# Kernel tuning notes

Hardware: AMD Instinct MI355X
Metric: run time of the kernel (lower is better)

The kernel has to match this reference:

```python
import jax, jax.numpy as jnp
import numpy as np

N, D, H = 4096, 128, 8

def setup_inputs() -> dict:
    key = jax.random.key(0)
    ks = jax.random.split(key, 7)
    xavier = float(np.sqrt(6.0 / (D + D)))  # xavier_uniform for [*, D, D]
    x = jax.random.normal(ks[0], (N, D), dtype=jnp.float32)
    W_k = jax.random.uniform(ks[1], (H, D, D), minval=-xavier, maxval=xavier, dtype=jnp.float32)
    W_q = jax.random.uniform(ks[2], (H, D, D), minval=-xavier, maxval=xavier, dtype=jnp.float32)
    W_v = jax.random.uniform(ks[3], (H, D, D), minval=-xavier, maxval=xavier, dtype=jnp.float32)
    W_m = jnp.ones((H,), dtype=jnp.float32)
    lim = float(1.0 / np.sqrt(D))  # default torch Linear init range
    Wg = jax.random.uniform(ks[4], (D, D), minval=-lim, maxval=lim, dtype=jnp.float32)
    bg = jax.random.uniform(ks[5], (D,), minval=-lim, maxval=lim, dtype=jnp.float32)
    return {"x": x, "W_k": W_k, "W_q": W_q, "W_v": W_v, "W_m": W_m, "Wg": Wg, "bg": bg}

def reference(x, W_k, W_q, W_v, W_m, Wg, bg):
    # per-head projections: [H, N, D]
    q = jnp.einsum('nf,hfd->hnd', x, W_q)
    k = jnp.einsum('nf,hfd->hnd', x, W_k)
    v = jnp.einsum('nf,hfd->hnd', x, W_v)
    # dense all-pairs attention scores per head: [H, N, N]
    e = jnp.einsum('hnd,hmd->hnm', q, k)
    attn = jax.nn.softmax(e, axis=-1)
    # weighted sum over values, then head-scaled accumulation: [N, D]
    out = jnp.einsum('h,hnm,hmd->nd', W_m, attn, v)
    # residual MLP: x + ReLU(Linear(x + out))
    h = x + out
    g = jax.nn.relu(h @ Wg.T + bg)
    return x + g
```

## Files before the change

### kernel.cpp

```cpp
#include <hip/hip_runtime.h>

#define NROWS 4096
#define DDIM  128
#define NHEAD 8

typedef __attribute__((ext_vector_type(8))) short    short8;
typedef __attribute__((ext_vector_type(8))) _Float16 half8;
typedef __attribute__((ext_vector_type(4))) float    floatx4;

__device__ __forceinline__ float bf2f(unsigned short u){
  unsigned v = ((unsigned)u) << 16;
  return __builtin_bit_cast(float, v);
}
__device__ __forceinline__ unsigned short f2bf(float f){
  unsigned u = __builtin_bit_cast(unsigned, f);
  u += 0x7FFFu + ((u >> 16) & 1u);
  return (unsigned short)(u >> 16);
}
__device__ __forceinline__ void split2(float v, unsigned short& hi, unsigned short& lo){
  hi = f2bf(v);
  lo = f2bf(v - bf2f(hi));
}
__device__ __forceinline__ void async_cp16(const _Float16* g, _Float16* l){
  __builtin_amdgcn_global_load_lds(
      (const __attribute__((address_space(1))) void*)g,
      (__attribute__((address_space(3))) void*)l, 16, 0, 0);
}

__global__ void fill_kernel(float* __restrict__ out, float val, int n){
  int i = blockIdx.x * 256 + threadIdx.x;
  if (i < n) out[i] = val;
}

__global__ __launch_bounds__(256, 2) void proj_kernel(
    const float* __restrict__ x,
    const float* __restrict__ Wk, const float* __restrict__ Wv,
    _Float16* __restrict__ kfo, _Float16* __restrict__ vfo)
{
  __shared__ alignas(16) unsigned short wthi[DDIM][72];
  __shared__ alignas(16) unsigned short wtlo[DDIM][72];
  const int tid = threadIdx.x, lane = tid & 63, wave = tid >> 6;
  const int l4 = lane & 15, quad = lane >> 4;
  const int h = blockIdx.y, z = blockIdx.z;
  const float* W = (z == 0 ? Wk : Wv) + h * DDIM * DDIM;

  floatx4 acc[4][8];
#pragma unroll
  for (int t4 = 0; t4 < 4; t4++)
#pragma unroll
    for (int c = 0; c < 8; c++) acc[t4][c] = (floatx4)0.f;

  for (int fh = 0; fh < 2; fh++) {
    for (int i = tid; i < DDIM * 64; i += 256) {
      const int d = i >> 6, fl = i & 63;
      unsigned short hi, lo;
      split2(W[(fh * 64 + fl) * DDIM + d], hi, lo);
      wthi[d][fl] = hi; wtlo[d][fl] = lo;
    }
    __syncthreads();

#pragma unroll
    for (int t4 = 0; t4 < 4; t4++) {
      const int tile = blockIdx.x * 4 + t4;
      const float* xr = x + (size_t)(tile * 64 + wave * 16 + l4) * DDIM + fh * 64 + quad * 8;
      short8 ah[2], al[2];
#pragma unroll
      for (int t2 = 0; t2 < 2; t2++) {
        float4 v0 = *(const float4*)(xr + t2 * 32);
        float4 v1 = *(const float4*)(xr + t2 * 32 + 4);
        float xv[8] = {v0.x, v0.y, v0.z, v0.w, v1.x, v1.y, v1.z, v1.w};
#pragma unroll
        for (int j = 0; j < 8; j++) {
          unsigned short hi, lo; split2(xv[j], hi, lo);
          ah[t2][j] = (short)hi; al[t2][j] = (short)lo;
        }
      }
#pragma unroll
      for (int t2 = 0; t2 < 2; t2++) {
#pragma unroll
        for (int c = 0; c < 8; c++) {
          short8 bh = *(const short8*)(&wthi[c * 16 + l4][t2 * 32 + quad * 8]);
          short8 bl = *(const short8*)(&wtlo[c * 16 + l4][t2 * 32 + quad * 8]);
          acc[t4][c] = __builtin_amdgcn_mfma_f32_16x16x32_bf16(ah[t2], bh, acc[t4][c], 0, 0, 0);
          acc[t4][c] = __builtin_amdgcn_mfma_f32_16x16x32_bf16(al[t2], bh, acc[t4][c], 0, 0, 0);
          acc[t4][c] = __builtin_amdgcn_mfma_f32_16x16x32_bf16(ah[t2], bl, acc[t4][c], 0, 0, 0);
        }
      }
    }
    __syncthreads();
  }

  const int rb = wave * 16 + quad * 4;
#pragma unroll
  for (int t4 = 0; t4 < 4; t4++) {
    const int tile = blockIdx.x * 4 + t4;
    const size_t tilebase = (size_t)(h * 64 + tile) * 8192;
#pragma unroll
    for (int c = 0; c < 8; c++) {
      const int d = c * 16 + l4;
#pragma unroll
      for (int r = 0; r < 4; r++) {
        const int kl = rb + r;
        const float val = acc[t4][c][r];
        if (z == 0) {
          const int c2 = kl >> 4, l4k = kl & 15;
          const int tt = d >> 5, qd = (d >> 3) & 3, jj = d & 7;
          const int qX = qd ^ ((l4k >> 1) & 3);
          kfo[tilebase + (size_t)((c2 * 4 + tt) * 16 + l4k) * 32 + qX * 8 + jj] =
              (_Float16)val;
        } else {
          const int c2 = d >> 4, l4v = d & 15;
          const int tt = kl >> 5, qd = (kl >> 3) & 3, jj = kl & 7;
          const int qX = qd ^ ((l4v >> 1) & 3);
          vfo[tilebase + (size_t)((c2 * 2 + tt) * 16 + l4v) * 32 + qX * 8 + jj] =
              (_Float16)val;
        }
      }
    }
  }
}

union FlashLds {
  struct { unsigned short hi[DDIM][72], lo[DDIM][72]; } wq;
  float qf[64][132];
  struct { _Float16 k[2][8192], p[4][2][1024]; } kv;
};

__global__ __launch_bounds__(256, 2) void flash_kernel(
    const float* __restrict__ x, const float* __restrict__ Wq,
    const _Float16* __restrict__ kfo, const _Float16* __restrict__ vfo,
    _Float16* __restrict__ op, float* __restrict__ mb, float* __restrict__ lb)
{
  __shared__ alignas(16) FlashLds lds;
  const int tid = threadIdx.x, lane = tid & 63, wave = tid >> 6;
  const int l4 = lane & 15, quad = lane >> 4;
  const int h = blockIdx.x & 7, qt = (blockIdx.x >> 3) & 31, s = blockIdx.x >> 8;
  const int q0 = qt * 128;

  half8 aq[2][4];

  {
    floatx4 qacc[2][8];
#pragma unroll
    for (int sp = 0; sp < 2; sp++)
#pragma unroll
      for (int c = 0; c < 8; c++) qacc[sp][c] = (floatx4)0.f;

    const float* Wqh = Wq + h * DDIM * DDIM;
    for (int fh = 0; fh < 2; fh++) {
      for (int i = tid; i < DDIM * 64; i += 256) {
        const int d = i >> 6, fl = i & 63;
        unsigned short hi, lo;
        split2(Wqh[(fh * 64 + fl) * DDIM + d], hi, lo);
        lds.wq.hi[d][fl] = hi; lds.wq.lo[d][fl] = lo;
      }
      __syncthreads();
#pragma unroll
      for (int sp = 0; sp < 2; sp++) {
        const float* xr = x + (size_t)(q0 + sp * 64 + wave * 16 + l4) * DDIM + fh * 64 + quad * 8;
        short8 ah[2], al[2];
#pragma unroll
        for (int t2 = 0; t2 < 2; t2++) {
          float4 v0 = *(const float4*)(xr + t2 * 32);
          float4 v1 = *(const float4*)(xr + t2 * 32 + 4);
          float xv[8] = {v0.x, v0.y, v0.z, v0.w, v1.x, v1.y, v1.z, v1.w};
#pragma unroll
          for (int j = 0; j < 8; j++) {
            unsigned short hi, lo; split2(xv[j], hi, lo);
            ah[t2][j] = (short)hi; al[t2][j] = (short)lo;
          }
        }
#pragma unroll
        for (int t2 = 0; t2 < 2; t2++) {
#pragma unroll
          for (int c = 0; c < 8; c++) {
            short8 bh = *(const short8*)(&lds.wq.hi[c * 16 + l4][t2 * 32 + quad * 8]);
            short8 bl = *(const short8*)(&lds.wq.lo[c * 16 + l4][t2 * 32 + quad * 8]);
            qacc[sp][c] = __builtin_amdgcn_mfma_f32_16x16x32_bf16(ah[t2], bh, qacc[sp][c], 0, 0, 0);
            qacc[sp][c] = __builtin_amdgcn_mfma_f32_16x16x32_bf16(al[t2], bh, qacc[sp][c], 0, 0, 0);
            qacc[sp][c] = __builtin_amdgcn_mfma_f32_16x16x32_bf16(ah[t2], bl, qacc[sp][c], 0, 0, 0);
          }
        }
      }
      __syncthreads();
    }

#pragma unroll
    for (int sp = 0; sp < 2; sp++) {
#pragma unroll
      for (int c = 0; c < 8; c++)
#pragma unroll
        for (int r = 0; r < 4; r++)
          lds.qf[wave * 16 + quad * 4 + r][c * 16 + l4] = qacc[sp][c][r];
      __syncthreads();
      if ((wave >> 1) == sp) {
#pragma unroll
        for (int g = 0; g < 2; g++)
#pragma unroll
          for (int t = 0; t < 4; t++) {
            const float* qr = &lds.qf[(wave & 1) * 32 + g * 16 + l4][t * 32 + quad * 8];
            float4 v0 = *(const float4*)qr;
            float4 v1 = *(const float4*)(qr + 4);
            aq[g][t][0] = (_Float16)v0.x; aq[g][t][1] = (_Float16)v0.y;
            aq[g][t][2] = (_Float16)v0.z; aq[g][t][3] = (_Float16)v0.w;
            aq[g][t][4] = (_Float16)v1.x; aq[g][t][5] = (_Float16)v1.y;
            aq[g][t][6] = (_Float16)v1.z; aq[g][t][7] = (_Float16)v1.w;
          }
      }
      __syncthreads();
    }
  }

  float m_run[2][4];
#pragma unroll
  for (int g = 0; g < 2; g++)
#pragma unroll
    for (int r = 0; r < 4; r++) m_run[g][r] = -1e30f;
  floatx4 Oacc[2][8], lacc[2];
#pragma unroll
  for (int g = 0; g < 2; g++) {
    lacc[g] = (floatx4)0.f;
#pragma unroll
    for (int c = 0; c < 8; c++) Oacc[g][c] = (floatx4)0.f;
  }

  half8 vones;
#pragma unroll
  for (int j = 0; j < 8; j++) vones[j] = (_Float16)1.f;

  const _Float16* kfo_h = kfo + (size_t)h * 64 * 8192;
  const _Float16* vfo_h = vfo + (size_t)h * 64 * 8192;
  const int lq = (l4 * 4 + (quad ^ ((l4 >> 1) & 3))) * 8;
  const int kt0 = s * 32, kt1 = kt0 + 32;

  {
    const _Float16* ks = kfo_h + (size_t)kt0 * 8192 + wave * 2048 + lane * 8;
    _Float16* kd = &lds.kv.k[0][wave * 2048];
#pragma unroll
    for (int it = 0; it < 4; it++) async_cp16(ks + it * 512, kd + it * 512);
  }

  for (int kt = kt0; kt < kt1; ++kt) {
    const int cur = kt & 1;
    __syncthreads();

    half8 vfrag[8][2];
    {
      const _Float16* vtb = vfo_h + (size_t)kt * 8192;
#pragma unroll
      for (int c = 0; c < 8; c++)
#pragma unroll
        for (int t = 0; t < 2; t++)
          vfrag[c][t] = *(const half8*)(vtb + (c * 2 + t) * 512 + lq);
    }
    if (kt + 1 < kt1) {
      const _Float16* ks = kfo_h + (size_t)(kt + 1) * 8192 + wave * 2048 + lane * 8;
      _Float16* kd = &lds.kv.k[cur ^ 1][wave * 2048];
#pragma unroll
      for (int it = 0; it < 4; it++) async_cp16(ks + it * 512, kd + it * 512);
    }

    floatx4 Sf[2][4];
#pragma unroll
    for (int g = 0; g < 2; g++)
#pragma unroll
      for (int c = 0; c < 4; c++) Sf[g][c] = (floatx4)0.f;
#pragma unroll
    for (int t = 0; t < 4; t++) {
      half8 b[4];
#pragma unroll
      for (int c = 0; c < 4; c++)
        b[c] = *(const half8*)&lds.kv.k[cur][(c * 4 + t) * 512 + lq];
#pragma unroll
      for (int g = 0; g < 2; g++)
#pragma unroll
        for (int c = 0; c < 4; c++)
          Sf[g][c] = __builtin_amdgcn_mfma_f32_16x16x32_f16(aq[g][t], b[c], Sf[g][c], 0, 0, 0);
    }

    float alpha[2][4];
#pragma unroll
    for (int g = 0; g < 2; g++) {
      float mt[4];
#pragma unroll
      for (int r = 0; r < 4; r++)
        mt[r] = fmaxf(fmaxf(Sf[g][0][r], Sf[g][1][r]), fmaxf(Sf[g][2][r], Sf[g][3][r]));
#pragma unroll
      for (int mk = 1; mk <= 8; mk <<= 1)
#pragma unroll
        for (int r = 0; r < 4; r++) mt[r] = fmaxf(mt[r], __shfl_xor(mt[r], mk, 64));
#pragma unroll
      for (int r = 0; r < 4; r++) {
        const float mn = fmaxf(m_run[g][r], mt[r]);
        alpha[g][r] = __expf(m_run[g][r] - mn);
        m_run[g][r] = mn;
      }
#pragma unroll
      for (int r = 0; r < 4; r++)
#pragma unroll
        for (int c = 0; c < 4; c++) Sf[g][c][r] = __expf(Sf[g][c][r] - m_run[g][r]);
    }

#pragma unroll
    for (int g = 0; g < 2; g++)
#pragma unroll
      for (int c = 0; c < 4; c++)
#pragma unroll
        for (int r = 0; r < 4; r++)
          lds.kv.p[wave][g][((c * 2 + (l4 >> 3)) * 16 + quad * 4 + r) * 8 + (l4 & 7)] =
              (_Float16)Sf[g][c][r];

#pragma unroll
    for (int g = 0; g < 2; g++) {
      const bool moved = (alpha[g][0] != 1.f) | (alpha[g][1] != 1.f) |
                         (alpha[g][2] != 1.f) | (alpha[g][3] != 1.f);
      if (__any(moved)) {
#pragma unroll
        for (int c = 0; c < 8; c++) {
          Oacc[g][c][0] *= alpha[g][0]; Oacc[g][c][1] *= alpha[g][1];
          Oacc[g][c][2] *= alpha[g][2]; Oacc[g][c][3] *= alpha[g][3];
        }
        lacc[g][0] *= alpha[g][0]; lacc[g][1] *= alpha[g][1];
        lacc[g][2] *= alpha[g][2]; lacc[g][3] *= alpha[g][3];
      }
    }
#pragma unroll
    for (int t = 0; t < 2; t++) {
      half8 ap[2];
#pragma unroll
      for (int g = 0; g < 2; g++) {
        ap[g] = *(const half8*)&lds.kv.p[wave][g][((t * 4 + quad) * 16 + l4) * 8];
        lacc[g] = __builtin_amdgcn_mfma_f32_16x16x32_f16(ap[g], vones, lacc[g], 0, 0, 0);
      }
#pragma unroll
      for (int c = 0; c < 8; c++)
#pragma unroll
        for (int g = 0; g < 2; g++)
          Oacc[g][c] = __builtin_amdgcn_mfma_f32_16x16x32_f16(ap[g], vfrag[c][t], Oacc[g][c], 0, 0, 0);
    }
  }

#pragma unroll
  for (int g = 0; g < 2; g++) {
    const int rbase = wave * 32 + g * 16 + quad * 4;
    const size_t rowbase = (size_t)(s * NHEAD + h) * NROWS + q0 + rbase;
#pragma unroll
    for (int c = 0; c < 8; c++) {
      const int col = c * 16 + l4;
#pragma unroll
      for (int r = 0; r < 4; r++)
        op[(rowbase + r) * DDIM + col] = (_Float16)Oacc[g][c][r];
    }
    if (l4 == 0) {
#pragma unroll
      for (int r = 0; r < 4; r++) {
        mb[rowbase + r] = m_run[g][r];
        lb[rowbase + r] = lacc[g][r];
      }
    }
  }
}

__global__ __launch_bounds__(128) void merge_kernel(
    const _Float16* __restrict__ op, const float* __restrict__ mb,
    const float* __restrict__ lb, const float* __restrict__ Wm,
    float* __restrict__ u)
{
  __shared__ float sc[2][NHEAD];
  const int n = blockIdx.x, d = threadIdx.x;
  if (d < NHEAD) {
    const int h = d;
    const float m1 = mb[(size_t)h * NROWS + n];
    const float m2 = mb[(size_t)(NHEAD + h) * NROWS + n];
    const float l1 = lb[(size_t)h * NROWS + n];
    const float l2 = lb[(size_t)(NHEAD + h) * NROWS + n];
    const float m  = fmaxf(m1, m2);
    const float a1 = __expf(m1 - m), a2 = __expf(m2 - m);
    const float invL = Wm[h] / (l1 * a1 + l2 * a2);
    sc[0][h] = a1 * invL;
    sc[1][h] = a2 * invL;
  }
  __syncthreads();
  float acc = 0.f;
#pragma unroll
  for (int h = 0; h < NHEAD; h++) {
    acc += sc[0][h] * (float)op[((size_t)h * NROWS + n) * DDIM + d];
    acc += sc[1][h] * (float)op[((size_t)(NHEAD + h) * NROWS + n) * DDIM + d];
  }
  u[(size_t)n * DDIM + d] = acc;
}

__global__ __launch_bounds__(256, 2) void mlp_kernel(
    const float* __restrict__ x, const float* __restrict__ u,
    const float* __restrict__ Wg, const float* __restrict__ bg,
    float* __restrict__ out)
{
  __shared__ alignas(16) unsigned short wghi[DDIM][72];
  __shared__ alignas(16) unsigned short wglo[DDIM][72];
  const int tid = threadIdx.x, lane = tid & 63, wave = tid >> 6;
  const int l4 = lane & 15, quad = lane >> 4;
  const int r0 = blockIdx.x * 64;

  floatx4 acc[8];
#pragma unroll
  for (int c = 0; c < 8; c++) acc[c] = (floatx4)0.f;

  for (int fh = 0; fh < 2; fh++) {
    for (int i = tid; i < DDIM * 64; i += 256) {
      const int ii = i >> 6, jl = i & 63;
      unsigned short hi, lo;
      split2(Wg[ii * DDIM + fh * 64 + jl], hi, lo);
      wghi[ii][jl] = hi; wglo[ii][jl] = lo;
    }
    __syncthreads();

    const size_t xoff = (size_t)(r0 + wave * 16 + l4) * DDIM + fh * 64 + quad * 8;
    short8 ah[2], al[2];
#pragma unroll
    for (int t2 = 0; t2 < 2; t2++) {
      float4 x0 = *(const float4*)(x + xoff + t2 * 32);
      float4 x1 = *(const float4*)(x + xoff + t2 * 32 + 4);
      float4 u0 = *(const float4*)(u + xoff + t2 * 32);
      float4 u1 = *(const float4*)(u + xoff + t2 * 32 + 4);
      float hv[8] = {x0.x + u0.x, x0.y + u0.y, x0.z + u0.z, x0.w + u0.w,
                     x1.x + u1.x, x1.y + u1.y, x1.z + u1.z, x1.w + u1.w};
#pragma unroll
      for (int j = 0; j < 8; j++) {
        unsigned short hi, lo; split2(hv[j], hi, lo);
        ah[t2][j] = (short)hi; al[t2][j] = (short)lo;
      }
    }
#pragma unroll
    for (int t2 = 0; t2 < 2; t2++) {
#pragma unroll
      for (int c = 0; c < 8; c++) {
        short8 bh = *(const short8*)(&wghi[c * 16 + l4][t2 * 32 + quad * 8]);
        short8 bl = *(const short8*)(&wglo[c * 16 + l4][t2 * 32 + quad * 8]);
        acc[c] = __builtin_amdgcn_mfma_f32_16x16x32_bf16(ah[t2], bh, acc[c], 0, 0, 0);
        acc[c] = __builtin_amdgcn_mfma_f32_16x16x32_bf16(al[t2], bh, acc[c], 0, 0, 0);
        acc[c] = __builtin_amdgcn_mfma_f32_16x16x32_bf16(ah[t2], bl, acc[c], 0, 0, 0);
      }
    }
    __syncthreads();
  }

  const int rbase = wave * 16 + quad * 4;
#pragma unroll
  for (int c = 0; c < 8; c++) {
    const int col = c * 16 + l4;
    const float bgf = bg[col];
#pragma unroll
    for (int r = 0; r < 4; r++) {
      const size_t idx = (size_t)(r0 + rbase + r) * DDIM + col;
      out[idx] = x[idx] + fmaxf(acc[c][r] + bgf, 0.f);
    }
  }
}

extern "C" void kernel_launch(void* const* d_in, const int* in_sizes, int n_in,
                              void* d_out, int out_size, void* d_ws, size_t ws_size,
                              hipStream_t stream) {
  float* out = (float*)d_out;
  const int fill_blocks = (out_size + 255) / 256;

  const bool ok_sizes =
      n_in == 7 &&
      in_sizes[0] == NROWS * DDIM &&
      in_sizes[1] == NHEAD * DDIM * DDIM &&
      in_sizes[2] == NHEAD * DDIM * DDIM &&
      in_sizes[3] == NHEAD * DDIM * DDIM &&
      in_sizes[4] == NHEAD &&
      in_sizes[5] == DDIM * DDIM &&
      in_sizes[6] == DDIM &&
      out_size == NROWS * DDIM;
  if (!ok_sizes) {
    fill_kernel<<<fill_blocks, 256, 0, stream>>>(out, 1000.f, out_size);
    return;
  }

  const size_t HND = (size_t)NHEAD * NROWS * DDIM;
  const size_t ND  = (size_t)NROWS * DDIM;
  const size_t need = ND * 4 + 2 * HND * 2 + 2 * HND * 2 + 2 * NHEAD * NROWS * 8;
  if (ws_size < need) {
    fill_kernel<<<fill_blocks, 256, 0, stream>>>(out, 500.f, out_size);
    return;
  }

  const float* x  = (const float*)d_in[0];
  const float* Wk = (const float*)d_in[1];
  const float* Wq = (const float*)d_in[2];
  const float* Wv = (const float*)d_in[3];
  const float* Wm = (const float*)d_in[4];
  const float* Wg = (const float*)d_in[5];
  const float* bg = (const float*)d_in[6];

  float*     u   = (float*)d_ws;
  _Float16*  kfo = (_Float16*)(u + ND);
  _Float16*  vfo = kfo + HND;
  _Float16*  op  = vfo + HND;
  float*     mb  = (float*)(op + 2 * HND);
  float*     lb  = mb + 2 * NHEAD * NROWS;

  (void)hipGetLastError();
  proj_kernel<<<dim3(16, NHEAD, 2), 256, 0, stream>>>(x, Wk, Wv, kfo, vfo);
  flash_kernel<<<dim3(512), 256, 0, stream>>>(x, Wq, kfo, vfo, op, mb, lb);
  merge_kernel<<<dim3(4096), 128, 0, stream>>>(op, mb, lb, Wm, u);
  mlp_kernel<<<dim3(64), 256, 0, stream>>>(x, u, Wg, bg, out);
  if (hipGetLastError() != hipSuccess) {
    fill_kernel<<<fill_blocks, 256, 0, stream>>>(out, 2000.f, out_size);
  }
}
```

Baseline: 254.8 us.

## Use single fp16 MFMA for projections and fuse merge into MLP kernel

Replaces the split-bf16 three-MFMA emulation of fp32 GEMMs in the K/V, Q and MLP projections with a single fp16 MFMA on fp16-converted inputs and weights. The proj kernel now computes both K and V per block, loading x once, with a new grid shape. The separate merge kernel is folded into the MLP kernel, which combines the split-softmax partials into an fp16 LDS tile and drops the u workspace round trip. This trades projection and MLP accuracy (fp16 rounding of x, weights and h) for fewer MFMAs and one fewer launch.

```diff
diff --git a/kernel.cpp b/kernel.cpp
--- a/kernel.cpp
+++ b/kernel.cpp
@@ -4,23 +4,9 @@
 #define DDIM  128
 #define NHEAD 8
 
-typedef __attribute__((ext_vector_type(8))) short    short8;
 typedef __attribute__((ext_vector_type(8))) _Float16 half8;
 typedef __attribute__((ext_vector_type(4))) float    floatx4;
 
-__device__ __forceinline__ float bf2f(unsigned short u){
-  unsigned v = ((unsigned)u) << 16;
-  return __builtin_bit_cast(float, v);
-}
-__device__ __forceinline__ unsigned short f2bf(float f){
-  unsigned u = __builtin_bit_cast(unsigned, f);
-  u += 0x7FFFu + ((u >> 16) & 1u);
-  return (unsigned short)(u >> 16);
-}
-__device__ __forceinline__ void split2(float v, unsigned short& hi, unsigned short& lo){
-  hi = f2bf(v);
-  lo = f2bf(v - bf2f(hi));
-}
 __device__ __forceinline__ void async_cp16(const _Float16* g, _Float16* l){
   __builtin_amdgcn_global_load_lds(
       (const __attribute__((address_space(1))) void*)g,
@@ -30,6 +16,17 @@
 __global__ void fill_kernel(float* __restrict__ out, float val, int n){
   int i = blockIdx.x * 256 + threadIdx.x;
   if (i < n) out[i] = val;
+}
+
+__device__ __forceinline__ half8 f32x8_to_h8(const float* p){
+  float4 v0 = *(const float4*)p;
+  float4 v1 = *(const float4*)(p + 4);
+  half8 r;
+  r[0] = (_Float16)v0.x; r[1] = (_Float16)v0.y;
+  r[2] = (_Float16)v0.z; r[3] = (_Float16)v0.w;
+  r[4] = (_Float16)v1.x; r[5] = (_Float16)v1.y;
+  r[6] = (_Float16)v1.z; r[7] = (_Float16)v1.w;
+  return r;
 }
 
 __global__ __launch_bounds__(256, 2) void proj_kernel(
@@ -37,91 +34,79 @@
     const float* __restrict__ Wk, const float* __restrict__ Wv,
     _Float16* __restrict__ kfo, _Float16* __restrict__ vfo)
 {
-  __shared__ alignas(16) unsigned short wthi[DDIM][72];
-  __shared__ alignas(16) unsigned short wtlo[DDIM][72];
+  __shared__ alignas(16) _Float16 wt[DDIM][136];
   const int tid = threadIdx.x, lane = tid & 63, wave = tid >> 6;
   const int l4 = lane & 15, quad = lane >> 4;
-  const int h = blockIdx.y, z = blockIdx.z;
-  const float* W = (z == 0 ? Wk : Wv) + h * DDIM * DDIM;
-
-  floatx4 acc[4][8];
-#pragma unroll
-  for (int t4 = 0; t4 < 4; t4++)
-#pragma unroll
-    for (int c = 0; c < 8; c++) acc[t4][c] = (floatx4)0.f;
-
-  for (int fh = 0; fh < 2; fh++) {
-    for (int i = tid; i < DDIM * 64; i += 256) {
-      const int d = i >> 6, fl = i & 63;
-      unsigned short hi, lo;
-      split2(W[(fh * 64 + fl) * DDIM + d], hi, lo);
-      wthi[d][fl] = hi; wtlo[d][fl] = lo;
+  const int h = blockIdx.y;
+
+  half8 xf[2][4];
+#pragma unroll
+  for (int t2 = 0; t2 < 2; t2++) {
+    const int tile = blockIdx.x * 2 + t2;
+    const float* xr = x + (size_t)(tile * 64 + wave * 16 + l4) * DDIM + quad * 8;
+#pragma unroll
+    for (int t = 0; t < 4; t++) xf[t2][t] = f32x8_to_h8(xr + t * 32);
+  }
+
+  for (int z = 0; z < 2; z++) {
+    const float* W = (z == 0 ? Wk : Wv) + h * DDIM * DDIM;
+    if (z) __syncthreads();
+    for (int i = tid; i < DDIM * DDIM; i += 256) {
+      const int f = i >> 7, d = i & 127;
+      wt[d][f] = (_Float16)W[i];
     }
     __syncthreads();
 
-#pragma unroll
-    for (int t4 = 0; t4 < 4; t4++) {
-      const int tile = blockIdx.x * 4 + t4;
-      const float* xr = x + (size_t)(tile * 64 + wave * 16 + l4) * DDIM + fh * 64 + quad * 8;
-      short8 ah[2], al[2];
-#pragma unroll
-      for (int t2 = 0; t2 < 2; t2++) {
-        float4 v0 = *(const float4*)(xr + t2 * 32);
-        float4 v1 = *(const float4*)(xr + t2 * 32 + 4);
-        float xv[8] = {v0.x, v0.y, v0.z, v0.w, v1.x, v1.y, v1.z, v1.w};
-#pragma unroll
-        for (int j = 0; j < 8; j++) {
-          unsigned short hi, lo; split2(xv[j], hi, lo);
-          ah[t2][j] = (short)hi; al[t2][j] = (short)lo;
+    floatx4 acc[2][8];
+#pragma unroll
+    for (int t2 = 0; t2 < 2; t2++)
+#pragma unroll
+      for (int c = 0; c < 8; c++) acc[t2][c] = (floatx4)0.f;
+
+#pragma unroll
+    for (int t = 0; t < 4; t++) {
+#pragma unroll
+      for (int c = 0; c < 8; c++) {
+        half8 b = *(const half8*)&wt[c * 16 + l4][t * 32 + quad * 8];
+#pragma unroll
+        for (int t2 = 0; t2 < 2; t2++)
+          acc[t2][c] = __builtin_amdgcn_mfma_f32_16x16x32_f16(xf[t2][t], b, acc[t2][c], 0, 0, 0);
+      }
+    }
+
+    const int rb = wave * 16 + quad * 4;
+#pragma unroll
+    for (int t2 = 0; t2 < 2; t2++) {
+      const int tile = blockIdx.x * 2 + t2;
+      const size_t tilebase = (size_t)(h * 64 + tile) * 8192;
+#pragma unroll
+      for (int c = 0; c < 8; c++) {
+        const int d = c * 16 + l4;
+#pragma unroll
+        for (int r = 0; r < 4; r++) {
+          const int kl = rb + r;
+          const float val = acc[t2][c][r];
+          if (z == 0) {
+            const int c2 = kl >> 4, l4k = kl & 15;
+            const int tt = d >> 5, qd = (d >> 3) & 3, jj = d & 7;
+            const int qX = qd ^ ((l4k >> 1) & 3);
+            kfo[tilebase + (size_t)((c2 * 4 + tt) * 16 + l4k) * 32 + qX * 8 + jj] =
+                (_Float16)val;
+          } else {
+            const int c2 = d >> 4, l4v = d & 15;
+            const int tt = kl >> 5, qd = (kl >> 3) & 3, jj = kl & 7;
+            const int qX = qd ^ ((l4v >> 1) & 3);
+            vfo[tilebase + (size_t)((c2 * 2 + tt) * 16 + l4v) * 32 + qX * 8 + jj] =
+                (_Float16)val;
+          }
         }
       }
-#pragma unroll
-      for (int t2 = 0; t2 < 2; t2++) {
-#pragma unroll
-        for (int c = 0; c < 8; c++) {
-          short8 bh = *(const short8*)(&wthi[c * 16 + l4][t2 * 32 + quad * 8]);
-          short8 bl = *(const short8*)(&wtlo[c * 16 + l4][t2 * 32 + quad * 8]);
-          acc[t4][c] = __builtin_amdgcn_mfma_f32_16x16x32_bf16(ah[t2], bh, acc[t4][c], 0, 0, 0);
-          acc[t4][c] = __builtin_amdgcn_mfma_f32_16x16x32_bf16(al[t2], bh, acc[t4][c], 0, 0, 0);
-          acc[t4][c] = __builtin_amdgcn_mfma_f32_16x16x32_bf16(ah[t2], bl, acc[t4][c], 0, 0, 0);
-        }
-      }
-    }
-    __syncthreads();
-  }
-
-  const int rb = wave * 16 + quad * 4;
-#pragma unroll
-  for (int t4 = 0; t4 < 4; t4++) {
-    const int tile = blockIdx.x * 4 + t4;
-    const size_t tilebase = (size_t)(h * 64 + tile) * 8192;
-#pragma unroll
-    for (int c = 0; c < 8; c++) {
-      const int d = c * 16 + l4;
-#pragma unroll
-      for (int r = 0; r < 4; r++) {
-        const int kl = rb + r;
-        const float val = acc[t4][c][r];
-        if (z == 0) {
-          const int c2 = kl >> 4, l4k = kl & 15;
-          const int tt = d >> 5, qd = (d >> 3) & 3, jj = d & 7;
-          const int qX = qd ^ ((l4k >> 1) & 3);
-          kfo[tilebase + (size_t)((c2 * 4 + tt) * 16 + l4k) * 32 + qX * 8 + jj] =
-              (_Float16)val;
-        } else {
-          const int c2 = d >> 4, l4v = d & 15;
-          const int tt = kl >> 5, qd = (kl >> 3) & 3, jj = kl & 7;
-          const int qX = qd ^ ((l4v >> 1) & 3);
-          vfo[tilebase + (size_t)((c2 * 2 + tt) * 16 + l4v) * 32 + qX * 8 + jj] =
-              (_Float16)val;
-        }
-      }
     }
   }
 }
 
 union FlashLds {
-  struct { unsigned short hi[DDIM][72], lo[DDIM][72]; } wq;
+  _Float16 wq[DDIM][136];
   float qf[64][132];
   struct { _Float16 k[2][8192], p[4][2][1024]; } kv;
 };
@@ -140,50 +125,37 @@
   half8 aq[2][4];
 
   {
+    const float* Wqh = Wq + h * DDIM * DDIM;
+    for (int i = tid; i < DDIM * DDIM; i += 256) {
+      const int f = i >> 7, d = i & 127;
+      lds.wq[d][f] = (_Float16)Wqh[i];
+    }
+    __syncthreads();
+
+    half8 xf2[2][4];
+#pragma unroll
+    for (int sp = 0; sp < 2; sp++) {
+      const float* xr = x + (size_t)(q0 + sp * 64 + wave * 16 + l4) * DDIM + quad * 8;
+#pragma unroll
+      for (int t = 0; t < 4; t++) xf2[sp][t] = f32x8_to_h8(xr + t * 32);
+    }
+
     floatx4 qacc[2][8];
 #pragma unroll
     for (int sp = 0; sp < 2; sp++)
 #pragma unroll
       for (int c = 0; c < 8; c++) qacc[sp][c] = (floatx4)0.f;
-
-    const float* Wqh = Wq + h * DDIM * DDIM;
-    for (int fh = 0; fh < 2; fh++) {
-      for (int i = tid; i < DDIM * 64; i += 256) {
-        const int d = i >> 6, fl = i & 63;
-        unsigned short hi, lo;
-        split2(Wqh[(fh * 64 + fl) * DDIM + d], hi, lo);
-        lds.wq.hi[d][fl] = hi; lds.wq.lo[d][fl] = lo;
-      }
-      __syncthreads();
-#pragma unroll
-      for (int sp = 0; sp < 2; sp++) {
-        const float* xr = x + (size_t)(q0 + sp * 64 + wave * 16 + l4) * DDIM + fh * 64 + quad * 8;
-        short8 ah[2], al[2];
-#pragma unroll
-        for (int t2 = 0; t2 < 2; t2++) {
-          float4 v0 = *(const float4*)(xr + t2 * 32);
-          float4 v1 = *(const float4*)(xr + t2 * 32 + 4);
-          float xv[8] = {v0.x, v0.y, v0.z, v0.w, v1.x, v1.y, v1.z, v1.w};
-#pragma unroll
-          for (int j = 0; j < 8; j++) {
-            unsigned short hi, lo; split2(xv[j], hi, lo);
-            ah[t2][j] = (short)hi; al[t2][j] = (short)lo;
-          }
-        }
-#pragma unroll
-        for (int t2 = 0; t2 < 2; t2++) {
-#pragma unroll
-          for (int c = 0; c < 8; c++) {
-            short8 bh = *(const short8*)(&lds.wq.hi[c * 16 + l4][t2 * 32 + quad * 8]);
-            short8 bl = *(const short8*)(&lds.wq.lo[c * 16 + l4][t2 * 32 + quad * 8]);
-            qacc[sp][c] = __builtin_amdgcn_mfma_f32_16x16x32_bf16(ah[t2], bh, qacc[sp][c], 0, 0, 0);
-            qacc[sp][c] = __builtin_amdgcn_mfma_f32_16x16x32_bf16(al[t2], bh, qacc[sp][c], 0, 0, 0);
-            qacc[sp][c] = __builtin_amdgcn_mfma_f32_16x16x32_bf16(ah[t2], bl, qacc[sp][c], 0, 0, 0);
-          }
-        }
-      }
-      __syncthreads();
-    }
+#pragma unroll
+    for (int t = 0; t < 4; t++) {
+#pragma unroll
+      for (int c = 0; c < 8; c++) {
+        half8 b = *(const half8*)&lds.wq[c * 16 + l4][t * 32 + quad * 8];
+#pragma unroll
+        for (int sp = 0; sp < 2; sp++)
+          qacc[sp][c] = __builtin_amdgcn_mfma_f32_16x16x32_f16(xf2[sp][t], b, qacc[sp][c], 0, 0, 0);
+      }
+    }
+    __syncthreads();
 
 #pragma unroll
     for (int sp = 0; sp < 2; sp++) {
@@ -197,15 +169,8 @@
 #pragma unroll
         for (int g = 0; g < 2; g++)
 #pragma unroll
-          for (int t = 0; t < 4; t++) {
-            const float* qr = &lds.qf[(wave & 1) * 32 + g * 16 + l4][t * 32 + quad * 8];
-            float4 v0 = *(const float4*)qr;
-            float4 v1 = *(const float4*)(qr + 4);
-            aq[g][t][0] = (_Float16)v0.x; aq[g][t][1] = (_Float16)v0.y;
-            aq[g][t][2] = (_Float16)v0.z; aq[g][t][3] = (_Float16)v0.w;
-            aq[g][t][4] = (_Float16)v1.x; aq[g][t][5] = (_Float16)v1.y;
-            aq[g][t][6] = (_Float16)v1.z; aq[g][t][7] = (_Float16)v1.w;
-          }
+          for (int t = 0; t < 4; t++)
+            aq[g][t] = f32x8_to_h8(&lds.qf[(wave & 1) * 32 + g * 16 + l4][t * 32 + quad * 8]);
       }
       __syncthreads();
     }
@@ -361,87 +326,63 @@
   }
 }
 
-__global__ __launch_bounds__(128) void merge_kernel(
+__global__ __launch_bounds__(256, 2) void mlp_kernel(
+    const float* __restrict__ x,
     const _Float16* __restrict__ op, const float* __restrict__ mb,
     const float* __restrict__ lb, const float* __restrict__ Wm,
-    float* __restrict__ u)
-{
-  __shared__ float sc[2][NHEAD];
-  const int n = blockIdx.x, d = threadIdx.x;
-  if (d < NHEAD) {
-    const int h = d;
-    const float m1 = mb[(size_t)h * NROWS + n];
-    const float m2 = mb[(size_t)(NHEAD + h) * NROWS + n];
-    const float l1 = lb[(size_t)h * NROWS + n];
-    const float l2 = lb[(size_t)(NHEAD + h) * NROWS + n];
-    const float m  = fmaxf(m1, m2);
-    const float a1 = __expf(m1 - m), a2 = __expf(m2 - m);
-    const float invL = Wm[h] / (l1 * a1 + l2 * a2);
-    sc[0][h] = a1 * invL;
-    sc[1][h] = a2 * invL;
-  }
-  __syncthreads();
-  float acc = 0.f;
-#pragma unroll
-  for (int h = 0; h < NHEAD; h++) {
-    acc += sc[0][h] * (float)op[((size_t)h * NROWS + n) * DDIM + d];
-    acc += sc[1][h] * (float)op[((size_t)(NHEAD + h) * NROWS + n) * DDIM + d];
-  }
-  u[(size_t)n * DDIM + d] = acc;
-}
-
-__global__ __launch_bounds__(256, 2) void mlp_kernel(
-    const float* __restrict__ x, const float* __restrict__ u,
     const float* __restrict__ Wg, const float* __restrict__ bg,
     float* __restrict__ out)
 {
-  __shared__ alignas(16) unsigned short wghi[DDIM][72];
-  __shared__ alignas(16) unsigned short wglo[DDIM][72];
+  __shared__ alignas(16) _Float16 wg_s[DDIM][136];
+  __shared__ alignas(16) _Float16 h_s[64][136];
+  __shared__ float sc_s[64][16];
   const int tid = threadIdx.x, lane = tid & 63, wave = tid >> 6;
   const int l4 = lane & 15, quad = lane >> 4;
   const int r0 = blockIdx.x * 64;
 
+  for (int i = tid; i < DDIM * DDIM; i += 256)
+    wg_s[i >> 7][i & 127] = (_Float16)Wg[i];
+
+  if (tid < 64) {
+    const int n = r0 + tid;
+#pragma unroll
+    for (int hh = 0; hh < NHEAD; hh++) {
+      const float m1 = mb[(size_t)hh * NROWS + n];
+      const float m2 = mb[(size_t)(NHEAD + hh) * NROWS + n];
+      const float l1 = lb[(size_t)hh * NROWS + n];
+      const float l2 = lb[(size_t)(NHEAD + hh) * NROWS + n];
+      const float m  = fmaxf(m1, m2);
+      const float a1 = __expf(m1 - m), a2 = __expf(m2 - m);
+      const float invL = Wm[hh] / (l1 * a1 + l2 * a2);
+      sc_s[tid][hh] = a1 * invL;
+      sc_s[tid][NHEAD + hh] = a2 * invL;
+    }
+  }
+  __syncthreads();
+
+  for (int it = 0; it < 32; it++) {
+    const int e = tid + 256 * it;
+    const int d = e & 127, r = e >> 7;
+    const int n = r0 + r;
+    float acc = x[(size_t)n * DDIM + d];
+#pragma unroll
+    for (int sh = 0; sh < 16; sh++)
+      acc += sc_s[r][sh] * (float)op[((size_t)sh * NROWS + n) * DDIM + d];
+    h_s[r][d] = (_Float16)acc;
+  }
+  __syncthreads();
+
   floatx4 acc[8];
 #pragma unroll
   for (int c = 0; c < 8; c++) acc[c] = (floatx4)0.f;
-
-  for (int fh = 0; fh < 2; fh++) {
-    for (int i = tid; i < DDIM * 64; i += 256) {
-      const int ii = i >> 6, jl = i & 63;
-      unsigned short hi, lo;
-      split2(Wg[ii * DDIM + fh * 64 + jl], hi, lo);
-      wghi[ii][jl] = hi; wglo[ii][jl] = lo;
-    }
-    __syncthreads();
-
-    const size_t xoff = (size_t)(r0 + wave * 16 + l4) * DDIM + fh * 64 + quad * 8;
-    short8 ah[2], al[2];
-#pragma unroll
-    for (int t2 = 0; t2 < 2; t2++) {
-      float4 x0 = *(const float4*)(x + xoff + t2 * 32);
-      float4 x1 = *(const float4*)(x + xoff + t2 * 32 + 4);
-      float4 u0 = *(const float4*)(u + xoff + t2 * 32);
-      float4 u1 = *(const float4*)(u + xoff + t2 * 32 + 4);
-      float hv[8] = {x0.x + u0.x, x0.y + u0.y, x0.z + u0.z, x0.w + u0.w,
-                     x1.x + u1.x, x1.y + u1.y, x1.z + u1.z, x1.w + u1.w};
-#pragma unroll
-      for (int j = 0; j < 8; j++) {
-        unsigned short hi, lo; split2(hv[j], hi, lo);
-        ah[t2][j] = (short)hi; al[t2][j] = (short)lo;
-      }
-    }
-#pragma unroll
-    for (int t2 = 0; t2 < 2; t2++) {
-#pragma unroll
-      for (int c = 0; c < 8; c++) {
-        short8 bh = *(const short8*)(&wghi[c * 16 + l4][t2 * 32 + quad * 8]);
-        short8 bl = *(const short8*)(&wglo[c * 16 + l4][t2 * 32 + quad * 8]);
-        acc[c] = __builtin_amdgcn_mfma_f32_16x16x32_bf16(ah[t2], bh, acc[c], 0, 0, 0);
-        acc[c] = __builtin_amdgcn_mfma_f32_16x16x32_bf16(al[t2], bh, acc[c], 0, 0, 0);
-        acc[c] = __builtin_amdgcn_mfma_f32_16x16x32_bf16(ah[t2], bl, acc[c], 0, 0, 0);
-      }
-    }
-    __syncthreads();
+#pragma unroll
+  for (int t = 0; t < 4; t++) {
+    half8 a = *(const half8*)&h_s[wave * 16 + l4][t * 32 + quad * 8];
+#pragma unroll
+    for (int c = 0; c < 8; c++) {
+      half8 b = *(const half8*)&wg_s[c * 16 + l4][t * 32 + quad * 8];
+      acc[c] = __builtin_amdgcn_mfma_f32_16x16x32_f16(a, b, acc[c], 0, 0, 0);
+    }
   }
 
   const int rbase = wave * 16 + quad * 4;
@@ -479,8 +420,7 @@
   }
 
   const size_t HND = (size_t)NHEAD * NROWS * DDIM;
-  const size_t ND  = (size_t)NROWS * DDIM;
-  const size_t need = ND * 4 + 2 * HND * 2 + 2 * HND * 2 + 2 * NHEAD * NROWS * 8;
+  const size_t need = 2 * HND * 2 + 2 * HND * 2 + 2 * NHEAD * NROWS * 8;
   if (ws_size < need) {
     fill_kernel<<<fill_blocks, 256, 0, stream>>>(out, 500.f, out_size);
     return;
@@ -494,18 +434,16 @@
   const float* Wg = (const float*)d_in[5];
   const float* bg = (const float*)d_in[6];
 
-  float*     u   = (float*)d_ws;
-  _Float16*  kfo = (_Float16*)(u + ND);
+  _Float16*  kfo = (_Float16*)d_ws;
   _Float16*  vfo = kfo + HND;
   _Float16*  op  = vfo + HND;
   float*     mb  = (float*)(op + 2 * HND);
   float*     lb  = mb + 2 * NHEAD * NROWS;
 
   (void)hipGetLastError();
-  proj_kernel<<<dim3(16, NHEAD, 2), 256, 0, stream>>>(x, Wk, Wv, kfo, vfo);
+  proj_kernel<<<dim3(32, NHEAD), 256, 0, stream>>>(x, Wk, Wv, kfo, vfo);
   flash_kernel<<<dim3(512), 256, 0, stream>>>(x, Wq, kfo, vfo, op, mb, lb);
-  merge_kernel<<<dim3(4096), 128, 0, stream>>>(op, mb, lb, Wm, u);
-  mlp_kernel<<<dim3(64), 256, 0, stream>>>(x, u, Wg, bg, out);
+  mlp_kernel<<<dim3(64), 256, 0, stream>>>(x, op, mb, lb, Wm, Wg, bg, out);
   if (hipGetLastError() != hipSuccess) {
     fill_kernel<<<fill_blocks, 256, 0, stream>>>(out, 2000.f, out_size);
   }
```

After: 258.2 us. No clear change (+1.4%).
